# Optimization experiments

Hardware: AMD Instinct MI355X
Metric: run time of the kernel (lower is better)

Reference implementation:

```python
import jax, jax.numpy as jnp
import numpy as np

HD_DIM = 4096
BUNDLE_SIZE = 128
STRIDE = 128  # bundle_size - overlap, overlap = 0
EPS = 1e-8


def setup_inputs() -> dict:
    key = jax.random.key(0)
    k1, k2 = jax.random.split(key)
    inputs = jax.random.normal(k1, (4, 2048, HD_DIM), dtype=jnp.float32)
    # base vector ~ N(0, 1/sqrt(hd_dim)) as in RandomNormal(stddev=1/sqrt(hd_dim))
    base = jax.random.normal(k2, (HD_DIM,), dtype=jnp.float32) / jnp.sqrt(jnp.float32(HD_DIM))
    # position_weights initialized to decay_rate**i
    pos_w = jnp.power(jnp.float32(0.99), jnp.arange(BUNDLE_SIZE, dtype=jnp.float32))
    return {"inputs": inputs, "bundle_position_base": base, "position_weights": pos_w}


def reference(inputs, bundle_position_base, position_weights):
    B, S, D = inputs.shape
    nb = (S - BUNDLE_SIZE) // STRIDE + 1  # number of bundles

    # Cyclic-shift position vectors: pos[s, d] = base[(d - s) mod D]
    shifts = jnp.arange(BUNDLE_SIZE)
    idx = jnp.mod(jnp.arange(D)[None, :] - shifts[:, None], D)  # [bs, D]
    pos = bundle_position_base[idx]                              # [bs, D]
    w = jax.nn.softmax(position_weights)                         # [bs]
    pos = pos * w[:, None]

    # overlap=0 and S divisible by bundle_size -> bundles tile the sequence
    tok = inputs.reshape(B, nb, BUNDLE_SIZE, D)  # [B, nb, bs, D]

    # circular correlation: real(ifft(fft(tok) * conj(fft(pos))))
    # both operands real -> use rfft/irfft (identical math, half the work)
    tok_f = jnp.fft.rfft(tok, axis=-1)                 # [B, nb, bs, D//2+1]
    pos_f = jnp.conj(jnp.fft.rfft(pos, axis=-1))       # [bs, D//2+1]
    bound = jnp.fft.irfft(tok_f * pos_f[None, None], n=D, axis=-1)  # [B, nb, bs, D]

    bundle = jnp.sum(bound, axis=2)  # [B, nb, D]
    # tf.nn.l2_normalize: x * rsqrt(max(sum(x^2), eps))
    ssq = jnp.sum(bundle * bundle, axis=-1, keepdims=True)
    return (bundle * jax.lax.rsqrt(jnp.maximum(ssq, EPS))).astype(jnp.float32)
```

## Files before the change

### kernel.cpp

```cpp
#include <hip/hip_runtime.h>

#define D 4096
#define DM 4095
#define BS 128
#define NROW 64
#define JC 8

#define ZSTR 520
#define PSTR 616
#define PBLEN 4736

typedef __attribute__((ext_vector_type(8))) short bf16x8;
typedef __attribute__((ext_vector_type(4))) float f32x4;

__device__ __forceinline__ unsigned short f2bf(float f) {
  union { float f; unsigned int u; } v;
  v.f = f;
  const unsigned int r = v.u + 0x7fffu + ((v.u >> 16) & 1u);
  return (unsigned short)(r >> 16);
}

__device__ __forceinline__ float bf2f(unsigned short h) {
  union { unsigned int u; float f; } v;
  v.u = (unsigned int)h << 16;
  return v.f;
}

__global__ __launch_bounds__(256) void zshift_k(const float* __restrict__ tok,
                                                const float* __restrict__ pw,
                                                const float* __restrict__ base,
                                                unsigned short* __restrict__ zb,
                                                unsigned short* __restrict__ pb) {
  const int t = threadIdx.x;
  const int mc = blockIdx.x;
  const int row = blockIdx.y;

  if (mc == 0 && row == 0) {
    for (int x = t; x < PBLEN; x += 256) pb[x] = f2bf(base[x & DM]);
  }

  __shared__ float wsh[BS];
  __shared__ float red[4];
  __shared__ float4 xsh[128];
  {
    const float v = (t < BS) ? pw[t] : -1e30f;
    float m = v;
#pragma unroll
    for (int o = 32; o > 0; o >>= 1) m = fmaxf(m, __shfl_xor(m, o));
    if ((t & 63) == 0) red[t >> 6] = m;
    __syncthreads();
    m = fmaxf(fmaxf(red[0], red[1]), fmaxf(red[2], red[3]));
    const float e = (t < BS) ? expf(v - m) : 0.f;
    float s = e;
#pragma unroll
    for (int o = 32; o > 0; o >>= 1) s += __shfl_xor(s, o);
    __syncthreads();
    if ((t & 63) == 0) red[t >> 6] = s;
    __syncthreads();
    s = red[0] + red[1] + red[2] + red[3];
    if (t < BS) wsh[t] = e / s;
    __syncthreads();
  }

  const int g = t & 127;
  const int h = t >> 7;
  const int og = (mc << 7) + g;
  const float4* tr = (const float4*)(tok + (size_t)row * (BS * D));

  float4 acc = make_float4(0.f, 0.f, 0.f, 0.f);
#pragma unroll
  for (int qq = 0; qq < 16; ++qq) {
    const int q = (h << 4) + qq;
    const float w0 = wsh[4 * q + 0], w1 = wsh[4 * q + 1];
    const float w2 = wsh[4 * q + 2], w3 = wsh[4 * q + 3];
    const int G = (og + q) & 1023;
    const int G1 = (G + 1) & 1023;
    const size_t r0 = (size_t)(4 * q + 0) << 10;
    const size_t r1 = (size_t)(4 * q + 1) << 10;
    const size_t r2 = (size_t)(4 * q + 2) << 10;
    const size_t r3 = (size_t)(4 * q + 3) << 10;
    const float4 a0 = tr[r0 + G];
    const float4 a1 = tr[r1 + G], b1 = tr[r1 + G1];
    const float4 a2 = tr[r2 + G], b2 = tr[r2 + G1];
    const float4 a3 = tr[r3 + G], b3 = tr[r3 + G1];
    acc.x += w0 * a0.x; acc.y += w0 * a0.y;
    acc.z += w0 * a0.z; acc.w += w0 * a0.w;
    acc.x += w1 * a1.y; acc.y += w1 * a1.z;
    acc.z += w1 * a1.w; acc.w += w1 * b1.x;
    acc.x += w2 * a2.z; acc.y += w2 * a2.w;
    acc.z += w2 * b2.x; acc.w += w2 * b2.y;
    acc.x += w3 * a3.w; acc.y += w3 * b3.x;
    acc.z += w3 * b3.y; acc.w += w3 * b3.z;
  }
  if (h) xsh[g] = acc;
  __syncthreads();
  if (!h) {
    const float4 o = xsh[g];
    ushort4 u;
    u.x = f2bf(acc.x + o.x);
    u.y = f2bf(acc.y + o.y);
    u.z = f2bf(acc.z + o.z);
    u.w = f2bf(acc.w + o.w);
    *(ushort4*)(zb + (size_t)row * D + ((size_t)og << 2)) = u;
  }
}

__global__ __launch_bounds__(256) void corr_k(const unsigned short* __restrict__ zb,
                                              const unsigned short* __restrict__ pb,
                                              unsigned short* __restrict__ braw) {
  __shared__ __align__(16) unsigned short zsh[16 * ZSTR];
  __shared__ __align__(16) unsigned short psh[8 * PSTR];
  const int t = threadIdx.x;
  const int jc = blockIdx.x;
  const int dg = blockIdx.y;
  const int rt = blockIdx.z;
  const int jb = jc << 9;
  const int d0b = dg << 6;

  {
    const int rr = t >> 4;
    const int c0 = (t & 15) << 5;
    const uint4* src =
        (const uint4*)(zb + (size_t)(rt * 16 + rr) * D + jb + c0);
    uint4* dst = (uint4*)(zsh + rr * ZSTR + c0);
    dst[0] = src[0];
    dst[1] = src[1];
    dst[2] = src[2];
    dst[3] = src[3];
  }
  {
    const int r = t >> 5;
    const int x0 = t & 31;
    const int sr = (jb - d0b - 64 + 2 * D + r) & DM;
    const unsigned short* src = pb + sr;
    unsigned short* dst = psh + r * PSTR;
    for (int x = x0; x < PSTR; x += 32) dst[x] = src[x];
  }
  __syncthreads();

  const int lane = t & 63;
  const int w = t >> 6;
  const int dd = lane & 15;
  const int q = lane >> 4;
  const int a0 = 64 + (q << 3) - (w << 4) - dd;
  const int pr = a0 & 7;
  const int px = a0 - pr;
  const unsigned short* pA = psh + pr * PSTR + px;
  const unsigned short* pB = zsh + dd * ZSTR + (q << 3);

  f32x4 acc = {0.f, 0.f, 0.f, 0.f};
#pragma unroll
  for (int ks = 0; ks < 16; ++ks) {
    const bf16x8 af = *(const bf16x8*)(pA + (ks << 5));
    const bf16x8 bf = *(const bf16x8*)(pB + (ks << 5));
    acc = __builtin_amdgcn_mfma_f32_16x16x32_bf16(af, bf, acc, 0, 0, 0);
  }
  const int row = rt * 16 + dd;
  const int d = d0b + (w << 4) + (q << 2);
  ushort4 u;
  u.x = f2bf(acc[0]);
  u.y = f2bf(acc[1]);
  u.z = f2bf(acc[2]);
  u.w = f2bf(acc[3]);
  *(ushort4*)(braw + (size_t)(jc * NROW + row) * D + d) = u;
}

__global__ __launch_bounds__(1024) void norm_k(const unsigned short* __restrict__ braw,
                                               float* __restrict__ out) {
  const int t = threadIdx.x;
  const int row = blockIdx.x;
  float4 s = make_float4(0.f, 0.f, 0.f, 0.f);
#pragma unroll
  for (int p = 0; p < JC; ++p) {
    const ushort4 v = *(const ushort4*)(braw +
        (size_t)(p * NROW + row) * D + (t << 2));
    s.x += bf2f(v.x); s.y += bf2f(v.y); s.z += bf2f(v.z); s.w += bf2f(v.w);
  }
  float ssq = s.x * s.x + s.y * s.y + s.z * s.z + s.w * s.w;
#pragma unroll
  for (int o = 32; o > 0; o >>= 1) ssq += __shfl_xor(ssq, o);
  __shared__ float red[16];
  if ((t & 63) == 0) red[t >> 6] = ssq;
  __syncthreads();
  float tot = 0.f;
#pragma unroll
  for (int i = 0; i < 16; ++i) tot += red[i];
  const float sc = rsqrtf(fmaxf(tot, 1e-8f));
  float4 o;
  o.x = s.x * sc; o.y = s.y * sc; o.z = s.z * sc; o.w = s.w * sc;
  ((float4*)out)[(size_t)row * (D / 4) + t] = o;
}

extern "C" void kernel_launch(void* const* d_in, const int* in_sizes, int n_in,
                              void* d_out, int out_size, void* d_ws, size_t ws_size,
                              hipStream_t stream) {
  (void)in_sizes; (void)n_in; (void)out_size; (void)ws_size;
  const float* tok = (const float*)d_in[0];
  const float* base = (const float*)d_in[1];
  const float* pw = (const float*)d_in[2];
  float* out = (float*)d_out;

  unsigned short* zb = (unsigned short*)d_ws;
  unsigned short* pb = zb + (size_t)NROW * D;
  unsigned short* braw = pb + 8192;

  zshift_k<<<dim3(8, NROW), 256, 0, stream>>>(tok, pw, base, zb, pb);
  corr_k<<<dim3(JC, 64, 4), 256, 0, stream>>>(zb, pb, braw);
  norm_k<<<NROW, 1024, 0, stream>>>(braw, out);
}
```

Before: 206.0 us.

## Reduce correlation chunks in-block and read operands directly from global memory

Result: slower. 222.0 us (+7.8%).

```diff
diff --git a/kernel.cpp b/kernel.cpp
--- a/kernel.cpp
+++ b/kernel.cpp
@@ -6,8 +6,6 @@
 #define NROW 64
 #define JC 8
 
-#define ZSTR 520
-#define PSTR 616
 #define PBLEN 4736
 
 typedef __attribute__((ext_vector_type(8))) short bf16x8;
@@ -30,13 +28,17 @@
                                                 const float* __restrict__ pw,
                                                 const float* __restrict__ base,
                                                 unsigned short* __restrict__ zb,
-                                                unsigned short* __restrict__ pb) {
+                                                unsigned short* __restrict__ pbp) {
   const int t = threadIdx.x;
   const int mc = blockIdx.x;
   const int row = blockIdx.y;
 
   if (mc == 0 && row == 0) {
-    for (int x = t; x < PBLEN; x += 256) pb[x] = f2bf(base[x & DM]);
+    for (int x = t; x < PBLEN; x += 256) {
+#pragma unroll
+      for (int p = 0; p < 8; ++p)
+        pbp[p * PBLEN + x] = f2bf(base[(p + x) & DM]);
+    }
   }
 
   __shared__ float wsh[BS];
@@ -105,78 +107,66 @@
   }
 }
 
-__global__ __launch_bounds__(256) void corr_k(const unsigned short* __restrict__ zb,
-                                              const unsigned short* __restrict__ pb,
-                                              unsigned short* __restrict__ braw) {
-  __shared__ __align__(16) unsigned short zsh[16 * ZSTR];
-  __shared__ __align__(16) unsigned short psh[8 * PSTR];
+__global__ __launch_bounds__(512) void corr_k(const unsigned short* __restrict__ zb,
+                                              const unsigned short* __restrict__ pbp,
+                                              float* __restrict__ bundle) {
   const int t = threadIdx.x;
-  const int jc = blockIdx.x;
-  const int dg = blockIdx.y;
-  const int rt = blockIdx.z;
-  const int jb = jc << 9;
+  const int dg = blockIdx.x;
+  const int rt = blockIdx.y;
   const int d0b = dg << 6;
-
-  {
-    const int rr = t >> 4;
-    const int c0 = (t & 15) << 5;
-    const uint4* src =
-        (const uint4*)(zb + (size_t)(rt * 16 + rr) * D + jb + c0);
-    uint4* dst = (uint4*)(zsh + rr * ZSTR + c0);
-    dst[0] = src[0];
-    dst[1] = src[1];
-    dst[2] = src[2];
-    dst[3] = src[3];
-  }
-  {
-    const int r = t >> 5;
-    const int x0 = t & 31;
-    const int sr = (jb - d0b - 64 + 2 * D + r) & DM;
-    const unsigned short* src = pb + sr;
-    unsigned short* dst = psh + r * PSTR;
-    for (int x = x0; x < PSTR; x += 32) dst[x] = src[x];
-  }
-  __syncthreads();
 
   const int lane = t & 63;
   const int w = t >> 6;
+  const int wq = w & 3;
+  const int kh = w >> 2;
   const int dd = lane & 15;
   const int q = lane >> 4;
-  const int a0 = 64 + (q << 3) - (w << 4) - dd;
+
+  const int a0 = 64 + (q << 3) - (wq << 4) - dd;
   const int pr = a0 & 7;
   const int px = a0 - pr;
-  const unsigned short* pA = psh + pr * PSTR + px;
-  const unsigned short* pB = zsh + dd * ZSTR + (q << 3);
-
-  f32x4 acc = {0.f, 0.f, 0.f, 0.f};
-#pragma unroll
-  for (int ks = 0; ks < 16; ++ks) {
-    const bf16x8 af = *(const bf16x8*)(pA + (ks << 5));
-    const bf16x8 bf = *(const bf16x8*)(pB + (ks << 5));
-    acc = __builtin_amdgcn_mfma_f32_16x16x32_bf16(af, bf, acc, 0, 0, 0);
-  }
-  const int row = rt * 16 + dd;
-  const int d = d0b + (w << 4) + (q << 2);
-  ushort4 u;
-  u.x = f2bf(acc[0]);
-  u.y = f2bf(acc[1]);
-  u.z = f2bf(acc[2]);
-  u.w = f2bf(acc[3]);
-  *(ushort4*)(braw + (size_t)(jc * NROW + row) * D + d) = u;
-}
-
-__global__ __launch_bounds__(1024) void norm_k(const unsigned short* __restrict__ braw,
+
+  const unsigned short* zrow = zb + (size_t)(rt * 16 + dd) * D + (q << 3);
+  const unsigned short* arow = pbp + pr * PBLEN + px;
+
+  f32x4 acc0 = {0.f, 0.f, 0.f, 0.f};
+  f32x4 acc1 = {0.f, 0.f, 0.f, 0.f};
+#pragma unroll
+  for (int jj = 0; jj < 4; ++jj) {
+    const int jc = (kh << 2) + jj;
+    const int jb = jc << 9;
+    const int s0m = (jb - d0b - 64 + 2 * D) & DM;
+    const unsigned short* pA = arow + s0m;
+    const unsigned short* pB = zrow + jb;
+#pragma unroll
+    for (int ks = 0; ks < 16; ks += 2) {
+      const bf16x8 af0 = *(const bf16x8*)(pA + (ks << 5));
+      const bf16x8 bf0 = *(const bf16x8*)(pB + (ks << 5));
+      acc0 = __builtin_amdgcn_mfma_f32_16x16x32_bf16(af0, bf0, acc0, 0, 0, 0);
+      const bf16x8 af1 = *(const bf16x8*)(pA + ((ks + 1) << 5));
+      const bf16x8 bf1 = *(const bf16x8*)(pB + ((ks + 1) << 5));
+      acc1 = __builtin_amdgcn_mfma_f32_16x16x32_bf16(af1, bf1, acc1, 0, 0, 0);
+    }
+  }
+  f32x4 acc = acc0 + acc1;
+
+  __shared__ f32x4 red[256];
+  if (kh) red[(wq << 6) + lane] = acc;
+  __syncthreads();
+  if (!kh) {
+    acc = acc + red[(wq << 6) + lane];
+    const int row = rt * 16 + dd;
+    const int d = d0b + (wq << 4) + (q << 2);
+    *(f32x4*)(bundle + (size_t)row * D + d) = acc;
+  }
+}
+
+__global__ __launch_bounds__(1024) void norm_k(const float* __restrict__ bundle,
                                                float* __restrict__ out) {
   const int t = threadIdx.x;
   const int row = blockIdx.x;
-  float4 s = make_float4(0.f, 0.f, 0.f, 0.f);
-#pragma unroll
-  for (int p = 0; p < JC; ++p) {
-    const ushort4 v = *(const ushort4*)(braw +
-        (size_t)(p * NROW + row) * D + (t << 2));
-    s.x += bf2f(v.x); s.y += bf2f(v.y); s.z += bf2f(v.z); s.w += bf2f(v.w);
-  }
-  float ssq = s.x * s.x + s.y * s.y + s.z * s.z + s.w * s.w;
+  const float4 v = ((const float4*)(bundle + (size_t)row * D))[t];
+  float ssq = v.x * v.x + v.y * v.y + v.z * v.z + v.w * v.w;
 #pragma unroll
   for (int o = 32; o > 0; o >>= 1) ssq += __shfl_xor(ssq, o);
   __shared__ float red[16];
@@ -186,9 +176,9 @@
 #pragma unroll
   for (int i = 0; i < 16; ++i) tot += red[i];
   const float sc = rsqrtf(fmaxf(tot, 1e-8f));
-  float4 o;
-  o.x = s.x * sc; o.y = s.y * sc; o.z = s.z * sc; o.w = s.w * sc;
-  ((float4*)out)[(size_t)row * (D / 4) + t] = o;
+  float4 o4;
+  o4.x = v.x * sc; o4.y = v.y * sc; o4.z = v.z * sc; o4.w = v.w * sc;
+  ((float4*)out)[(size_t)row * (D / 4) + t] = o4;
 }
 
 extern "C" void kernel_launch(void* const* d_in, const int* in_sizes, int n_in,
@@ -198,13 +188,14 @@
   const float* tok = (const float*)d_in[0];
   const float* base = (const float*)d_in[1];
   const float* pw = (const float*)d_in[2];
+
   float* out = (float*)d_out;
 
   unsigned short* zb = (unsigned short*)d_ws;
-  unsigned short* pb = zb + (size_t)NROW * D;
-  unsigned short* braw = pb + 8192;
-
-  zshift_k<<<dim3(8, NROW), 256, 0, stream>>>(tok, pw, base, zb, pb);
-  corr_k<<<dim3(JC, 64, 4), 256, 0, stream>>>(zb, pb, braw);
-  norm_k<<<NROW, 1024, 0, stream>>>(braw, out);
-}
+  unsigned short* pbp = zb + (size_t)NROW * D;
+  float* bundle = (float*)(pbp + 8 * PBLEN);
+
+  zshift_k<<<dim3(8, NROW), 256, 0, stream>>>(tok, pw, base, zb, pbp);
+  corr_k<<<dim3(64, 4), 512, 0, stream>>>(zb, pbp, bundle);
+  norm_k<<<NROW, 1024, 0, stream>>>(bundle, out);
+}
```
